# Kernel tuning notes

Measured on AMD Instinct MI355X. Metric: run time of the kernel, lower is better.

The kernel has to match this reference:

```python
import math
import jax, jax.numpy as jnp
import numpy as np

P = 1024
P_R = 128
A_MIN, A_MAX = 0.01, 0.995
TAU_INIT = 64.0
EPS = 1e-06
B, T = 8, 4096


def _xavier(key, shape):
    fan_in, fan_out = shape[0], shape[1]
    lim = math.sqrt(6.0 / (fan_in + fan_out))
    return jax.random.uniform(key, shape, jnp.float32, -lim, lim)


def setup_inputs() -> dict:
    key = jax.random.key(0)
    k_t, k_f, k_vr, k_vb, k_vo, k_wl = jax.random.split(key, 6)
    a0 = math.exp(-1.0 / max(TAU_INIT, 1.0))
    logit_a0 = math.log(a0 / (1.0 - a0 + 1e-09))
    return {
        "t": jax.random.normal(k_t, (B, T, P), jnp.float32),
        "F": jax.random.uniform(k_f, (B, T, P), jnp.float32),
        "V_r": _xavier(k_vr, (P, P_R)),
        "V_b": _xavier(k_vb, (P, P_R)),
        "V_o": _xavier(k_vo, (P_R, P)),
        "W_lambda": 0.02 * jax.random.normal(k_wl, (P_R, P_R), jnp.float32),
        "b_lambda": jnp.full((P_R,), logit_a0, jnp.float32),
    }


def reference(t, F, V_r, V_b, V_o, W_lambda, b_lambda):
    t = t.astype(jnp.float32)
    F = jax.lax.stop_gradient(F.astype(jnp.float32))  # F is detached in the original
    scale = 1.0 / math.sqrt(P_R)

    # decay gates: a = clamp(sigmoid((t @ V_r) @ W_lambda + b_lambda))  -> (B,T,P_r)
    r = jnp.einsum('btp,pr->btr', t, V_r)
    a = jax.nn.sigmoid(jnp.einsum('btr,rs->bts', r, W_lambda) + b_lambda)
    a = jnp.clip(a, A_MIN, A_MAX)

    # input drive: u = (F * t) @ V_b * scale  -> (B,T,P_r)
    u = jnp.einsum('btp,pr->btr', F * t, V_b) * scale

    def step(s, inp):
        a_i, u_i = inp                      # (B,P_r)
        s = a_i * s + u_i
        denom = jnp.sqrt(jnp.mean(s * s, axis=-1, keepdims=True) + EPS)
        s = s / denom
        return s, s

    s0 = jnp.zeros((t.shape[0], P_R), jnp.float32)
    _, s_seq = jax.lax.scan(step, s0, (jnp.swapaxes(a, 0, 1), jnp.swapaxes(u, 0, 1)))
    s = jnp.swapaxes(s_seq, 0, 1)           # (B,T,P_r)

    t_tilde = jnp.einsum('btr,rp->btp', s, V_o) + t  # residual=True
    new_cache = s[:, -1, :]
    return t_tilde, new_cache
```

## Files before the change

### kernel.cpp

```cpp
#include <hip/hip_runtime.h>
#include <math.h>

#define P_DIM 1024
#define R_DIM 128
#define B_DIM 8
#define T_DIM 4096
#define NROWS (B_DIM*T_DIM)

__global__ __launch_bounds__(256, 2) void stage1_kernel(
    const float* __restrict__ tin, const float* __restrict__ Fin,
    const float* __restrict__ Vr, const float* __restrict__ Vb,
    const float* __restrict__ Wl, const float* __restrict__ bl,
    float* __restrict__ au_ws, float* __restrict__ usq_ws)
{
    __shared__ float tA[32][36];
    __shared__ float tF[32][36];
    __shared__ float Bs[2][32][128];
    __shared__ float rS[32][132];

    const int tid  = threadIdx.x;
    const int c    = tid & 31;
    const int ry   = tid >> 5;
    const int row0 = blockIdx.x * 32;

    float accR[4][4] = {};
    float accU[4][4] = {};

    const int lr = tid >> 3;
    const int lk = (tid & 7) << 2;

    for (int k0 = 0; k0 < P_DIM; k0 += 32) {
        __syncthreads();
        float4 tv = *(const float4*)(tin + (long)(row0 + lr) * P_DIM + k0 + lk);
        float4 fv = *(const float4*)(Fin + (long)(row0 + lr) * P_DIM + k0 + lk);
        fv.x *= tv.x; fv.y *= tv.y; fv.z *= tv.z; fv.w *= tv.w;
        *(float4*)&tA[lr][lk] = tv;
        *(float4*)&tF[lr][lk] = fv;
#pragma unroll
        for (int i = 0; i < 4; i++) {
            int idx = tid + i * 256;
            ((float4*)&Bs[0][0][0])[idx] = ((const float4*)(Vr + (long)k0 * R_DIM))[idx];
            ((float4*)&Bs[1][0][0])[idx] = ((const float4*)(Vb + (long)k0 * R_DIM))[idx];
        }
        __syncthreads();
#pragma unroll
        for (int kk = 0; kk < 32; kk++) {
            float4 vr = *(const float4*)&Bs[0][kk][c * 4];
            float4 vb = *(const float4*)&Bs[1][kk][c * 4];
#pragma unroll
            for (int i = 0; i < 4; i++) {
                float ta = tA[ry * 4 + i][kk];
                float tf = tF[ry * 4 + i][kk];
                accR[i][0] = fmaf(ta, vr.x, accR[i][0]);
                accR[i][1] = fmaf(ta, vr.y, accR[i][1]);
                accR[i][2] = fmaf(ta, vr.z, accR[i][2]);
                accR[i][3] = fmaf(ta, vr.w, accR[i][3]);
                accU[i][0] = fmaf(tf, vb.x, accU[i][0]);
                accU[i][1] = fmaf(tf, vb.y, accU[i][1]);
                accU[i][2] = fmaf(tf, vb.z, accU[i][2]);
                accU[i][3] = fmaf(tf, vb.w, accU[i][3]);
            }
        }
    }

#pragma unroll
    for (int i = 0; i < 4; i++) {
        *(float4*)&rS[ry * 4 + i][c * 4] =
            make_float4(accR[i][0], accR[i][1], accR[i][2], accR[i][3]);
    }

    float4 bl4 = *(const float4*)(bl + c * 4);
    float z[4][4];
#pragma unroll
    for (int i = 0; i < 4; i++) { z[i][0] = bl4.x; z[i][1] = bl4.y; z[i][2] = bl4.z; z[i][3] = bl4.w; }

    for (int kc = 0; kc < R_DIM; kc += 32) {
        __syncthreads();
#pragma unroll
        for (int i2 = 0; i2 < 4; i2++) {
            int idx = tid + i2 * 256;
            ((float4*)&Bs[0][0][0])[idx] = ((const float4*)(Wl + (long)kc * R_DIM))[idx];
        }
        __syncthreads();
#pragma unroll
        for (int kk = 0; kk < 32; kk++) {
            float4 w = *(const float4*)&Bs[0][kk][c * 4];
#pragma unroll
            for (int i = 0; i < 4; i++) {
                float rv = rS[ry * 4 + i][kc + kk];
                z[i][0] = fmaf(rv, w.x, z[i][0]);
                z[i][1] = fmaf(rv, w.y, z[i][1]);
                z[i][2] = fmaf(rv, w.z, z[i][2]);
                z[i][3] = fmaf(rv, w.w, z[i][3]);
            }
        }
    }

    const float uscale = 0.08838834764831845f;
#pragma unroll
    for (int i = 0; i < 4; i++) {
        int row = row0 + ry * 4 + i;
        float4 av;
        av.x = fminf(fmaxf(1.f / (1.f + expf(-z[i][0])), 0.01f), 0.995f);
        av.y = fminf(fmaxf(1.f / (1.f + expf(-z[i][1])), 0.01f), 0.995f);
        av.z = fminf(fmaxf(1.f / (1.f + expf(-z[i][2])), 0.01f), 0.995f);
        av.w = fminf(fmaxf(1.f / (1.f + expf(-z[i][3])), 0.01f), 0.995f);
        float4 uv = make_float4(accU[i][0] * uscale, accU[i][1] * uscale,
                                accU[i][2] * uscale, accU[i][3] * uscale);
        float* dst = au_ws + ((long)row << 8) + c * 8;
        *(float4*)dst       = make_float4(av.x, av.y, uv.x, uv.y);
        *(float4*)(dst + 4) = make_float4(av.z, av.w, uv.z, uv.w);
        float us = fmaf(uv.x, uv.x, fmaf(uv.y, uv.y, fmaf(uv.z, uv.z, uv.w * uv.w)));
        us += __shfl_xor(us, 1);
        us += __shfl_xor(us, 2);
        us += __shfl_xor(us, 4);
        us += __shfl_xor(us, 8);
        us += __shfl_xor(us, 16);
        if (c == 0) usq_ws[row] = us;
    }
}

template <int CTRL, int ROW_MASK>
__device__ __forceinline__ float dpp_add(float x) {
    int xi = __float_as_int(x);
    int yi = __builtin_amdgcn_update_dpp(0, xi, CTRL, ROW_MASK, 0xf, false);
    return x + __int_as_float(yi);
}

__device__ __forceinline__ float wave64_sum(float x) {
    x = dpp_add<0xB1,  0xf>(x);
    x = dpp_add<0x4E,  0xf>(x);
    x = dpp_add<0x141, 0xf>(x);
    x = dpp_add<0x140, 0xf>(x);
    x = dpp_add<0x142, 0xa>(x);
    x = dpp_add<0x143, 0xc>(x);
    return __int_as_float(__builtin_amdgcn_readlane(__float_as_int(x), 63));
}

#define PF 16

__global__ __launch_bounds__(64) void scan_kernel(
    const float* __restrict__ au,
    const float* __restrict__ usq,
    float* __restrict__ s_ws,
    float* __restrict__ cache_out)
{
    const int b = blockIdx.x;
    const int lane = threadIdx.x;
    const long rowbase = (long)b * T_DIM;
    const float* usq_b = usq + rowbase;
    const float* au_b  = au + (rowbase << 8) + lane * 4;
    float*       s_b   = s_ws + (rowbase << 7) + lane * 2;

    float4 buf[PF];
    float  cq[PF];
#pragma unroll
    for (int j = 0; j < PF; j++) {
        buf[j] = *(const float4*)(au_b + ((long)j << 8));
        cq[j]  = usq_b[j];
    }

    float2 v   = make_float2(0.f, 0.f);
    float invp = 0.f;
    float Ap = 0.f, Bp = 0.f, Cp = 0.f;

    for (int i0 = 0; i0 < T_DIM; i0 += PF) {
#pragma unroll
        for (int j = 0; j < PF; j++) {
            const int i = i0 + j;
            float4 x = buf[j];
            float  C = cq[j];
            int ip = i + PF; if (ip > T_DIM - 1) ip = T_DIM - 1;
            buf[j] = *(const float4*)(au_b + ((long)ip << 8));
            cq[j]  = usq_b[ip];

            float px = x.x * v.x;
            float py = x.y * v.y;
            float pa = fmaf(px, px, py * py);
            float pb = fmaf(px, x.z, py * x.w);
            float A = wave64_sum(pa);
            float B = wave64_sum(pb);

            float tot = fmaf(invp * invp, Ap, fmaf(invp + invp, Bp, Cp));
            tot = fmaxf(tot, 0.f);
            float inv = rsqrtf(fmaf(tot, 0.0078125f, 1e-6f));

            int iw = (i > 0) ? i - 1 : 0;
            *(float2*)(s_b + ((long)iw << 7)) =
                make_float2(inv * v.x, inv * v.y);

            v.x = fmaf(inv, px, x.z);
            v.y = fmaf(inv, py, x.w);

            invp = inv; Ap = A; Bp = B; Cp = C;
        }
    }

    float tot = fmaf(invp * invp, Ap, fmaf(invp + invp, Bp, Cp));
    tot = fmaxf(tot, 0.f);
    float inv = rsqrtf(fmaf(tot, 0.0078125f, 1e-6f));
    float2 sfin = make_float2(inv * v.x, inv * v.y);
    *(float2*)(s_b + ((long)(T_DIM - 1) << 7)) = sfin;
    *(float2*)(cache_out + b * R_DIM + lane * 2) = sfin;
}

__global__ __launch_bounds__(256, 2) void stage3_kernel(
    const float* __restrict__ s_ws, const float* __restrict__ Vo,
    const float* __restrict__ tin, float* __restrict__ out)
{
    __shared__ float sS[16][128];
    __shared__ float VoS[32][256];

    const int tid = threadIdx.x;
    const int cb = blockIdx.x & 3;
    const int rb = blockIdx.x >> 2;
    const int row0 = rb * 16;
    const int col0 = cb * 256;
    const int tx = tid & 63;
    const int ty = tid >> 6;

    float acc[4][4] = {};

#pragma unroll
    for (int i = 0; i < 2; i++) {
        int idx = tid + i * 256;
        ((float4*)&sS[0][0])[idx] = *(const float4*)(s_ws + (long)row0 * R_DIM + idx * 4);
    }

    for (int k0 = 0; k0 < R_DIM; k0 += 32) {
        __syncthreads();
#pragma unroll
        for (int i = 0; i < 8; i++) {
            int idx = tid + i * 256;
            int r = idx >> 6;
            int cq = idx & 63;
            *(float4*)&VoS[r][cq * 4] =
                *(const float4*)(Vo + (long)(k0 + r) * P_DIM + col0 + cq * 4);
        }
        __syncthreads();
#pragma unroll
        for (int kk = 0; kk < 32; kk++) {
            float4 w = *(const float4*)&VoS[kk][tx * 4];
#pragma unroll
            for (int i = 0; i < 4; i++) {
                float sv = sS[ty * 4 + i][k0 + kk];
                acc[i][0] = fmaf(sv, w.x, acc[i][0]);
                acc[i][1] = fmaf(sv, w.y, acc[i][1]);
                acc[i][2] = fmaf(sv, w.z, acc[i][2]);
                acc[i][3] = fmaf(sv, w.w, acc[i][3]);
            }
        }
    }

#pragma unroll
    for (int i = 0; i < 4; i++) {
        int row = row0 + ty * 4 + i;
        float4 tv = *(const float4*)(tin + (long)row * P_DIM + col0 + tx * 4);
        float4 o = make_float4(acc[i][0] + tv.x, acc[i][1] + tv.y,
                               acc[i][2] + tv.z, acc[i][3] + tv.w);
        *(float4*)(out + (long)row * P_DIM + col0 + tx * 4) = o;
    }
}

extern "C" void kernel_launch(void* const* d_in, const int* in_sizes, int n_in,
                              void* d_out, int out_size, void* d_ws, size_t ws_size,
                              hipStream_t stream) {
    const float* t  = (const float*)d_in[0];
    const float* F  = (const float*)d_in[1];
    const float* Vr = (const float*)d_in[2];
    const float* Vb = (const float*)d_in[3];
    const float* Vo = (const float*)d_in[4];
    const float* Wl = (const float*)d_in[5];
    const float* bl = (const float*)d_in[6];
    float* out = (float*)d_out;

    float* au_ws  = (float*)d_ws;
    float* usq_ws = au_ws + (long)NROWS * 256;
    float* s_ws   = usq_ws + NROWS;

    hipLaunchKernelGGL(stage1_kernel, dim3(NROWS / 32), dim3(256), 0, stream,
                       t, F, Vr, Vb, Wl, bl, au_ws, usq_ws);
    hipLaunchKernelGGL(scan_kernel, dim3(B_DIM), dim3(64), 0, stream,
                       au_ws, usq_ws, s_ws, out + (long)NROWS * P_DIM);
    hipLaunchKernelGGL(stage3_kernel, dim3((NROWS / 16) * 4), dim3(256), 0, stream,
                       s_ws, Vo, t, out);
}
```

Before: 1.089 ms.

## Stream scan inputs through an LDS ring via async global-to-LDS loads

The scan kernel now prefetches the interleaved a/u rows with global_load_lds into a 32-slot shared-memory ring, 16 rows ahead. It uses explicit vmcnt waits and inline-asm stores in place of the previous 16-entry register prefetch. The per-row sum of u squared is now a third wave reduction inside the scan, so stage1 no longer computes it and the usq workspace array is gone. This is meant to cut register pressure and load-issue overhead on the serial critical path. The extra reduction may add latency per step, and the hand-counted vmcnt values must stay correct.

```diff
diff --git a/kernel.cpp b/kernel.cpp
--- a/kernel.cpp
+++ b/kernel.cpp
@@ -11,7 +11,7 @@
     const float* __restrict__ tin, const float* __restrict__ Fin,
     const float* __restrict__ Vr, const float* __restrict__ Vb,
     const float* __restrict__ Wl, const float* __restrict__ bl,
-    float* __restrict__ au_ws, float* __restrict__ usq_ws)
+    float* __restrict__ au_ws)
 {
     __shared__ float tA[32][36];
     __shared__ float tF[32][36];
@@ -110,13 +110,6 @@
         float* dst = au_ws + ((long)row << 8) + c * 8;
         *(float4*)dst       = make_float4(av.x, av.y, uv.x, uv.y);
         *(float4*)(dst + 4) = make_float4(av.z, av.w, uv.z, uv.w);
-        float us = fmaf(uv.x, uv.x, fmaf(uv.y, uv.y, fmaf(uv.z, uv.z, uv.w * uv.w)));
-        us += __shfl_xor(us, 1);
-        us += __shfl_xor(us, 2);
-        us += __shfl_xor(us, 4);
-        us += __shfl_xor(us, 8);
-        us += __shfl_xor(us, 16);
-        if (c == 0) usq_ws[row] = us;
     }
 }
 
@@ -137,67 +130,77 @@
     return __int_as_float(__builtin_amdgcn_readlane(__float_as_int(x), 63));
 }
 
-#define PF 16
+__device__ __forceinline__ void dma16(const float* gp, float* lp) {
+    __builtin_amdgcn_global_load_lds(
+        (const __attribute__((address_space(1))) void*)gp,
+        (__attribute__((address_space(3))) void*)lp, 16, 0, 0);
+}
+
+#define SCAN_WAIT(n) do {                                        \
+    asm volatile("s_waitcnt vmcnt(" #n ")" ::: "memory");        \
+    __builtin_amdgcn_sched_barrier(0);                           \
+} while (0)
+#define SCAN_STORE2(ptr, val) \
+    asm volatile("global_store_dwordx2 %0, %1, off" :: "v"(ptr), "v"(val) : "memory")
+
+#define SCAN_STEP(i_, n) do {                                                 \
+    SCAN_WAIT(n);                                                             \
+    float4 xn = *(const float4*)&sm[((i_) + 1) & 31][lane * 4];               \
+    dma16(au_g + ((long)((i_) + 16) << 8), &sm[((i_) + 16) & 31][0]);         \
+    float px = xa.x * v.x;                                                    \
+    float py = xa.y * v.y;                                                    \
+    float pa = fmaf(px, px, py * py);                                         \
+    float pb = fmaf(px, xa.z, py * xa.w);                                     \
+    float pc = fmaf(xa.z, xa.z, xa.w * xa.w);                                 \
+    float A  = wave64_sum(pa);                                                \
+    float Bv = wave64_sum(pb);                                                \
+    float Cv = wave64_sum(pc);                                                \
+    float tot = fmaxf(fmaf(i2p, Ap, fmaf(idp, Bp, Cp)), 0.f);                 \
+    float inv = rsqrtf(fmaf(tot, 0.0078125f, 1e-6f));                         \
+    float2 sv = make_float2(inv * v.x, inv * v.y);                            \
+    int iw_ = ((i_) > 0) ? (i_) - 1 : 0;                                      \
+    SCAN_STORE2(s_b + ((long)iw_ << 7), sv);                                  \
+    v.x = fmaf(inv, px, xa.z);                                                \
+    v.y = fmaf(inv, py, xa.w);                                                \
+    i2p = inv * inv; idp = inv + inv;                                         \
+    Ap = A; Bp = Bv; Cp = Cv;                                                 \
+    xa = xn;                                                                  \
+} while (0)
 
 __global__ __launch_bounds__(64) void scan_kernel(
     const float* __restrict__ au,
-    const float* __restrict__ usq,
     float* __restrict__ s_ws,
     float* __restrict__ cache_out)
 {
+    __shared__ float sm[32][256];
+
     const int b = blockIdx.x;
     const int lane = threadIdx.x;
     const long rowbase = (long)b * T_DIM;
-    const float* usq_b = usq + rowbase;
-    const float* au_b  = au + (rowbase << 8) + lane * 4;
-    float*       s_b   = s_ws + (rowbase << 7) + lane * 2;
-
-    float4 buf[PF];
-    float  cq[PF];
-#pragma unroll
-    for (int j = 0; j < PF; j++) {
-        buf[j] = *(const float4*)(au_b + ((long)j << 8));
-        cq[j]  = usq_b[j];
-    }
+    const float* au_g = au + (rowbase << 8) + lane * 4;
+    float*       s_b  = s_ws + (rowbase << 7) + lane * 2;
+
+#pragma unroll
+    for (int j = 0; j < 16; ++j)
+        dma16(au_g + ((long)j << 8), &sm[j][0]);
 
     float2 v   = make_float2(0.f, 0.f);
-    float invp = 0.f;
+    float i2p = 0.f, idp = 0.f;
     float Ap = 0.f, Bp = 0.f, Cp = 0.f;
 
-    for (int i0 = 0; i0 < T_DIM; i0 += PF) {
-#pragma unroll
-        for (int j = 0; j < PF; j++) {
-            const int i = i0 + j;
-            float4 x = buf[j];
-            float  C = cq[j];
-            int ip = i + PF; if (ip > T_DIM - 1) ip = T_DIM - 1;
-            buf[j] = *(const float4*)(au_b + ((long)ip << 8));
-            cq[j]  = usq_b[ip];
-
-            float px = x.x * v.x;
-            float py = x.y * v.y;
-            float pa = fmaf(px, px, py * py);
-            float pb = fmaf(px, x.z, py * x.w);
-            float A = wave64_sum(pa);
-            float B = wave64_sum(pb);
-
-            float tot = fmaf(invp * invp, Ap, fmaf(invp + invp, Bp, Cp));
-            tot = fmaxf(tot, 0.f);
-            float inv = rsqrtf(fmaf(tot, 0.0078125f, 1e-6f));
-
-            int iw = (i > 0) ? i - 1 : 0;
-            *(float2*)(s_b + ((long)iw << 7)) =
-                make_float2(inv * v.x, inv * v.y);
-
-            v.x = fmaf(inv, px, x.z);
-            v.y = fmaf(inv, py, x.w);
-
-            invp = inv; Ap = A; Bp = B; Cp = C;
-        }
-    }
-
-    float tot = fmaf(invp * invp, Ap, fmaf(invp + invp, Bp, Cp));
-    tot = fmaxf(tot, 0.f);
+    SCAN_WAIT(15);
+    float4 xa = *(const float4*)&sm[0][lane * 4];
+
+    SCAN_STEP(0, 14);  SCAN_STEP(1, 15);  SCAN_STEP(2, 16);  SCAN_STEP(3, 17);
+    SCAN_STEP(4, 18);  SCAN_STEP(5, 19);  SCAN_STEP(6, 20);  SCAN_STEP(7, 21);
+    SCAN_STEP(8, 22);  SCAN_STEP(9, 23);  SCAN_STEP(10, 24); SCAN_STEP(11, 25);
+    SCAN_STEP(12, 26); SCAN_STEP(13, 27); SCAN_STEP(14, 28);
+
+    for (int i = 15; i < T_DIM; ++i) {
+        SCAN_STEP(i, 29);
+    }
+
+    float tot = fmaxf(fmaf(i2p, Ap, fmaf(idp, Bp, Cp)), 0.f);
     float inv = rsqrtf(fmaf(tot, 0.0078125f, 1e-6f));
     float2 sfin = make_float2(inv * v.x, inv * v.y);
     *(float2*)(s_b + ((long)(T_DIM - 1) << 7)) = sfin;
@@ -274,14 +277,13 @@
     const float* bl = (const float*)d_in[6];
     float* out = (float*)d_out;
 
-    float* au_ws  = (float*)d_ws;
-    float* usq_ws = au_ws + (long)NROWS * 256;
-    float* s_ws   = usq_ws + NROWS;
+    float* au_ws = (float*)d_ws;
+    float* s_ws  = au_ws + (long)NROWS * 256;
 
     hipLaunchKernelGGL(stage1_kernel, dim3(NROWS / 32), dim3(256), 0, stream,
-                       t, F, Vr, Vb, Wl, bl, au_ws, usq_ws);
+                       t, F, Vr, Vb, Wl, bl, au_ws);
     hipLaunchKernelGGL(scan_kernel, dim3(B_DIM), dim3(64), 0, stream,
-                       au_ws, usq_ws, s_ws, out + (long)NROWS * P_DIM);
+                       au_ws, s_ws, out + (long)NROWS * P_DIM);
     hipLaunchKernelGGL(stage3_kernel, dim3((NROWS / 16) * 4), dim3(256), 0, stream,
                        s_ws, Vo, t, out);
 }
```

Measured after the change: 1.645 ms. +51.1%, slower.
